# Optimization experiments

Hardware: AMD Instinct MI355X
Metric: run time of the kernel (lower is better)

Reference implementation:

```python
import jax, jax.numpy as jnp
import numpy as np

EPS = 1e-05


def layer_norm(x, scale):
    # Faithful to source bug: returns scale * x_norm + scale (shift param unused)
    mean = jnp.mean(x, axis=-1, keepdims=True)
    var = jnp.var(x, axis=-1, keepdims=True)  # unbiased=False
    x_norm = (x - mean) / jnp.sqrt(var + EPS)
    return scale * x_norm + scale


def mhsa(x, wq, wk, wv, wo, bo, n_heads):
    b, t, d = x.shape
    hd = d // n_heads
    # torch Linear: y = x @ W.T (no qkv bias)
    q = (x @ wq.T).reshape(b, t, n_heads, hd).transpose(0, 2, 1, 3)  # bhtd
    k = (x @ wk.T).reshape(b, t, n_heads, hd).transpose(0, 2, 1, 3)
    v = (x @ wv.T).reshape(b, t, n_heads, hd).transpose(0, 2, 1, 3)
    scores = jnp.einsum('bhqd,bhkd->bhqk', q, k)
    causal = jnp.triu(jnp.ones((t, t), dtype=bool), k=1)
    scores = jnp.where(causal, -jnp.inf, scores)
    attn = jax.nn.softmax(scores / np.sqrt(hd).astype(np.float32), axis=-1)
    ctx = jnp.einsum('bhqk,bhkd->bhqd', attn, v)
    ctx = ctx.transpose(0, 2, 1, 3).reshape(b, t, d)
    return ctx @ wo.T + bo


def setup_inputs() -> dict:
    key = jax.random.key(0)
    ks = jax.random.split(key, 6)
    B, T, D = 2, 2048, 1024
    return {
        'x': jax.random.normal(ks[0], (B, T, D), dtype=jnp.float32),
        'wq': jax.random.normal(ks[1], (D, D), dtype=jnp.float32) * 0.02,
        'wk': jax.random.normal(ks[2], (D, D), dtype=jnp.float32) * 0.02,
        'wv': jax.random.normal(ks[3], (D, D), dtype=jnp.float32) * 0.02,
        'wo': jax.random.normal(ks[4], (D, D), dtype=jnp.float32) * 0.02,
        'bo': jnp.zeros((D,), dtype=jnp.float32),
        'ln1_scale': jnp.ones((D,), dtype=jnp.float32),
        'ln2_scale': jnp.ones((D,), dtype=jnp.float32),
    }


def reference(x, wq, wk, wv, wo, bo, ln1_scale, ln2_scale):
    n_heads = 16
    # Block 1: norm1 -> attn -> (+residual); dropout is identity in eval mode
    h = x + mhsa(layer_norm(x, ln1_scale), wq, wk, wv, wo, bo, n_heads)
    # Block 2: source calls self.attn (same weights) again, not self.ff
    out = h + mhsa(layer_norm(h, ln2_scale), wq, wk, wv, wo, bo, n_heads)
    return out
```

## Files before the change

### kernel.cpp

```cpp
#include <hip/hip_runtime.h>
#include <hip/hip_bf16.h>
#include <math.h>

#define Dm 1024
#define Tm 2048
#define Bm 2
#define Hm 16
#define HDm 64
#define Rm (Bm*Tm)
#define QKS 2048

typedef __attribute__((ext_vector_type(8))) short sh8;
typedef __attribute__((ext_vector_type(4))) float f32x4;

#define AS1(p) ((const __attribute__((address_space(1))) void*)(p))
#define AS3(p) ((__attribute__((address_space(3))) void*)(p))

__device__ __forceinline__ short f2bs(float f) {
    union { float f; unsigned u; } v; v.f = f;
    unsigned r = v.u + 0x7FFFu + ((v.u >> 16) & 1u);
    return (short)(r >> 16);
}

__global__ __launch_bounds__(256) void convert_w(const float* __restrict__ wq,
                                                 const float* __restrict__ wk,
                                                 const float* __restrict__ wv,
                                                 const float* __restrict__ wo,
                                                 short* __restrict__ wqkv,
                                                 short* __restrict__ wob) {
    int idx = (blockIdx.x * 256 + threadIdx.x) * 4;
    const int M1 = 1 << 20;
    const float* src; short* dst; int off;
    if (idx < M1)           { src = wq; dst = wqkv;          off = idx; }
    else if (idx < 2*M1)    { src = wk; dst = wqkv + M1;     off = idx - M1; }
    else if (idx < 3*M1)    { src = wv; dst = wqkv + 2*M1;   off = idx - 2*M1; }
    else                    { src = wo; dst = wob;           off = idx - 3*M1; }
    float4 v = *(const float4*)(src + off);
    short4 o;
    o.x = f2bs(v.x); o.y = f2bs(v.y); o.z = f2bs(v.z); o.w = f2bs(v.w);
    *(short4*)(dst + off) = o;
}

__global__ __launch_bounds__(256) void ln_kernel(const float* __restrict__ x,
                                                 const float* __restrict__ scale,
                                                 short* __restrict__ out) {
    int row = blockIdx.x;
    int t = threadIdx.x;
    const float4* xr = (const float4*)(x + (size_t)row * Dm);
    float4 v = xr[t];
    float s  = v.x + v.y + v.z + v.w;
    float ss = v.x*v.x + v.y*v.y + v.z*v.z + v.w*v.w;
    #pragma unroll
    for (int off = 32; off; off >>= 1) {
        s  += __shfl_xor(s, off);
        ss += __shfl_xor(ss, off);
    }
    __shared__ float red[8];
    int wave = t >> 6, lane = t & 63;
    if (lane == 0) { red[wave*2] = s; red[wave*2+1] = ss; }
    __syncthreads();
    s  = red[0] + red[2] + red[4] + red[6];
    ss = red[1] + red[3] + red[5] + red[7];
    float mean = s * (1.0f / Dm);
    float var  = ss * (1.0f / Dm) - mean * mean;
    float rstd = 1.0f / sqrtf(var + 1e-5f);
    float4 sc = ((const float4*)scale)[t];
    short4 o;
    o.x = f2bs(sc.x * ((v.x - mean) * rstd) + sc.x);
    o.y = f2bs(sc.y * ((v.y - mean) * rstd) + sc.y);
    o.z = f2bs(sc.z * ((v.z - mean) * rstd) + sc.z);
    o.w = f2bs(sc.w * ((v.w - mean) * rstd) + sc.w);
    ((short4*)(out + (size_t)row * Dm))[t] = o;
}

template<int BN, int MODE>
__global__ __launch_bounds__(256) void gemm_mfma(const short* __restrict__ A,
                                                 const short* __restrict__ B,
                                                 const float* __restrict__ bias,
                                                 const float* __restrict__ res,
                                                 void* __restrict__ Cv,
                                                 short* __restrict__ Vt,
                                                 int M, int N, int K) {
    __shared__ short As[128*32];
    __shared__ short Bs[BN*32];
    __shared__ short Tb[(MODE==1) ? 4*16*68 : 4];
    const int NJ = BN / 32;
    int t = threadIdx.x;
    int lane = t & 63, w = t >> 6;
    int l = lane & 15, quad = lane >> 4;
    int wm = (w & 1) * 64, wn = (w >> 1) * (BN/2);
    int m0 = blockIdx.y * 128, n0 = blockIdx.x * BN;

    f32x4 acc[4][NJ];
    #pragma unroll
    for (int i = 0; i < 4; i++)
        #pragma unroll
        for (int j = 0; j < NJ; j++)
            acc[i][j] = (f32x4){0.f,0.f,0.f,0.f};

    for (int k0 = 0; k0 < K; k0 += 32) {
        __syncthreads();
        #pragma unroll
        for (int p = 0; p < 2; p++) {
            int off = p*4096 + t*16;
            int row = off >> 6;
            int c = ((off >> 4) & 3) ^ (row & 3);
            const short* ga = A + (size_t)(m0 + row) * K + k0 + c*8;
            __builtin_amdgcn_global_load_lds(AS1(ga), AS3((char*)As + off), 16, 0, 0);
        }
        #pragma unroll
        for (int p = 0; p < BN/64; p++) {
            int off = p*4096 + t*16;
            int row = off >> 6;
            int c = ((off >> 4) & 3) ^ (row & 3);
            const short* gb = B + (size_t)(n0 + row) * K + k0 + c*8;
            __builtin_amdgcn_global_load_lds(AS1(gb), AS3((char*)Bs + off), 16, 0, 0);
        }
        __syncthreads();
        sh8 af[4], bf[NJ];
        #pragma unroll
        for (int i = 0; i < 4; i++) {
            int m = wm + i*16 + l;
            af[i] = *(const sh8*)((const char*)As + m*64 + ((quad ^ (m & 3)) * 16));
        }
        #pragma unroll
        for (int j = 0; j < NJ; j++) {
            int n = wn + j*16 + l;
            bf[j] = *(const sh8*)((const char*)Bs + n*64 + ((quad ^ (n & 3)) * 16));
        }
        #pragma unroll
        for (int i = 0; i < 4; i++)
            #pragma unroll
            for (int j = 0; j < NJ; j++)
                acc[i][j] = __builtin_amdgcn_mfma_f32_16x16x32_bf16(af[i], bf[j], acc[i][j], 0, 0, 0);
    }
    if (MODE == 0) {
        #pragma unroll
        for (int i = 0; i < 4; i++)
            #pragma unroll
            for (int j = 0; j < NJ; j++)
                #pragma unroll
                for (int r = 0; r < 4; r++) {
                    int m = m0 + wm + i*16 + quad*4 + r;
                    int n = n0 + wn + j*16 + l;
                    float vv = acc[i][j][r] + bias[n] + res[(size_t)m * N + n];
                    ((float*)Cv)[(size_t)m * N + n] = vv;
                }
    } else {
        if (n0 < 2048) {
            #pragma unroll
            for (int i = 0; i < 4; i++)
                #pragma unroll
                for (int j = 0; j < NJ; j++)
                    #pragma unroll
                    for (int r = 0; r < 4; r++) {
                        int m = m0 + wm + i*16 + quad*4 + r;
                        int n = n0 + wn + j*16 + l;
                        ((short*)Cv)[(size_t)m * QKS + n] = f2bs(acc[i][j][r]);
                    }
        } else {
            int bq = m0 >> 11;
            int key0 = (m0 & 2047) + wm;
            int h = (n0 + wn - 2048) >> 6;
            short* vout = Vt + ((size_t)(bq*Hm + h) * HDm) * Tm + key0;
            #pragma unroll
            for (int j = 0; j < NJ; j++) {
                #pragma unroll
                for (int i = 0; i < 4; i++) {
                    short4 o;
                    o.x = f2bs(acc[i][j][0]); o.y = f2bs(acc[i][j][1]);
                    o.z = f2bs(acc[i][j][2]); o.w = f2bs(acc[i][j][3]);
                    *(short4*)&Tb[w*(16*68) + l*68 + i*16 + quad*4] = o;
                }
                #pragma unroll
                for (int st = 0; st < 2; st++) {
                    int rr = st*8 + (lane >> 3);
                    int cc = lane & 7;
                    sh8 vv = *(const sh8*)&Tb[w*(16*68) + rr*68 + cc*8];
                    *(sh8*)(vout + (size_t)(j*16 + rr) * Tm + cc*8) = vv;
                }
            }
        }
    }
}

__device__ __forceinline__ void stage_kv(const short* kp0, const short* vh,
                                         int kbase, short* Kd, short* Vd, int t) {
    #pragma unroll
    for (int p = 0; p < 2; p++) {
        int off = p*4096 + t*16;
        int row = off >> 7;
        int c = ((off >> 4) & 7) ^ (row & 7);
        const short* gk = kp0 + (size_t)(kbase + row) * QKS + c*8;
        __builtin_amdgcn_global_load_lds(AS1(gk), AS3((char*)Kd + off), 16, 0, 0);
        const short* gv = vh + (size_t)row * Tm + kbase + c*8;
        __builtin_amdgcn_global_load_lds(AS1(gv), AS3((char*)Vd + off), 16, 0, 0);
    }
}

__global__ __launch_bounds__(256) void attn_mfma(const short* __restrict__ qk,
                                                 const short* __restrict__ vtg,
                                                 short* __restrict__ ctx) {
    __shared__ short Kl[2][64*64];
    __shared__ short Vl[2][64*64];
    __shared__ short Pl[4][16*64];
    int t = threadIdx.x;
    int lane = t & 63, w = t >> 6;
    int l = lane & 15, quad = lane >> 4;
    int bh = blockIdx.x;
    int xi = blockIdx.y;
    int cc0 = xi & 7, kk0 = xi >> 3;
    int qt = (kk0 == 0) ? cc0 : (kk0 == 1) ? (15 - cc0)
           : (kk0 == 2) ? (16 + cc0) : (31 - cc0);
    int b = bh >> 4, h = bh & 15;
    size_t rbase = (size_t)b * Tm;
    const short* qp0 = qk + rbase * QKS + h*HDm;
    const short* kp0 = qp0 + Dm;
    const short* vh  = vtg + ((size_t)bh * HDm) * Tm;
    int qtbase = qt * 64;

    sh8 qf0, qf1;
    {
        const short* qp = qp0 + (size_t)(qtbase + w*16 + l) * QKS + quad*8;
        qf0 = *(const sh8*)qp;
        qf1 = *(const sh8*)(qp + 32);
    }
    f32x4 O[4] = {{0,0,0,0},{0,0,0,0},{0,0,0,0},{0,0,0,0}};
    float ps[4] = {0.f, 0.f, 0.f, 0.f};

    int cur = 0;
    stage_kv(kp0, vh, 0, Kl[0], Vl[0], t);
    __syncthreads();

    int swl = l & 7;
    for (int kc = 0; kc <= qt; kc++) {
        int kbase = kc * 64;
        if (kc < qt)
            stage_kv(kp0, vh, kbase + 64, Kl[cur^1], Vl[cur^1], t);

        f32x4 S[4];
        #pragma unroll
        for (int kt = 0; kt < 4; kt++) {
            const f32x4 z = {0.f,0.f,0.f,0.f};
            int key = kt*16 + l;
            const char* kb = (const char*)Kl[cur] + key*128;
            int sw = key & 7;
            sh8 k0 = *(const sh8*)(kb + ((quad ^ sw) * 16));
            sh8 k1 = *(const sh8*)(kb + (((4 + quad) ^ sw) * 16));
            f32x4 s = __builtin_amdgcn_mfma_f32_16x16x32_bf16(k0, qf0, z, 0, 0, 0);
            s = __builtin_amdgcn_mfma_f32_16x16x32_bf16(k1, qf1, s, 0, 0, 0);
            S[kt] = s;
        }
        bool needmask = (kbase + 63 > qtbase + w*16);
        int qrow = qtbase + w*16 + l;
        #pragma unroll
        for (int kt = 0; kt < 4; kt++) {
            float p[4];
            if (needmask) {
                #pragma unroll
                for (int r = 0; r < 4; r++) {
                    int key = kbase + kt*16 + quad*4 + r;
                    p[r] = (key > qrow) ? 0.f : __expf(S[kt][r] * 0.125f);
                }
            } else {
                #pragma unroll
                for (int r = 0; r < 4; r++)
                    p[r] = __expf(S[kt][r] * 0.125f);
            }
            ps[kt] += (p[0] + p[1]) + (p[2] + p[3]);
            __hip_bfloat162 pa = __float22bfloat162_rn({p[0], p[1]});
            __hip_bfloat162 pb = __float22bfloat162_rn({p[2], p[3]});
            union { __hip_bfloat162 hh[2]; short4 s4; } u;
            u.hh[0] = pa; u.hh[1] = pb;
            int g = (kt*2 + (quad >> 1)) ^ swl;
            *(short4*)&Pl[w][l*64 + g*8 + (quad & 1)*4] = u.s4;
        }
        sh8 p0 = *(const sh8*)&Pl[w][l*64 + ((quad ^ swl) * 8)];
        sh8 p1 = *(const sh8*)&Pl[w][l*64 + (((4 + quad) ^ swl) * 8)];
        #pragma unroll
        for (int dt = 0; dt < 4; dt++) {
            int d = dt*16 + l;
            const char* vb = (const char*)Vl[cur] + d*128;
            int sw = d & 7;
            sh8 v0 = *(const sh8*)(vb + ((quad ^ sw) * 16));
            sh8 v1 = *(const sh8*)(vb + (((4 + quad) ^ sw) * 16));
            O[dt] = __builtin_amdgcn_mfma_f32_16x16x32_bf16(p0, v0, O[dt], 0, 0, 0);
            O[dt] = __builtin_amdgcn_mfma_f32_16x16x32_bf16(p1, v1, O[dt], 0, 0, 0);
        }
        __syncthreads();
        cur ^= 1;
    }

    float psum = (ps[0] + ps[1]) + (ps[2] + ps[3]);
    psum += __shfl_xor(psum, 16);
    psum += __shfl_xor(psum, 32);
    #pragma unroll
    for (int r = 0; r < 4; r++) {
        int src = (lane & 48) | (((lane >> 4) << 2) + r);
        float inv = 1.0f / __shfl(psum, src);
        int row = qtbase + w*16 + quad*4 + r;
        #pragma unroll
        for (int dt = 0; dt < 4; dt++)
            ctx[(rbase + row) * Dm + h*HDm + dt*16 + l] = f2bs(O[dt][r] * inv);
    }
}

extern "C" void kernel_launch(void* const* d_in, const int* in_sizes, int n_in,
                              void* d_out, int out_size, void* d_ws, size_t ws_size,
                              hipStream_t stream) {
    const float* x   = (const float*)d_in[0];
    const float* wq  = (const float*)d_in[1];
    const float* wk  = (const float*)d_in[2];
    const float* wv  = (const float*)d_in[3];
    const float* wo  = (const float*)d_in[4];
    const float* bo  = (const float*)d_in[5];
    const float* ln1 = (const float*)d_in[6];
    const float* ln2 = (const float*)d_in[7];
    float* out = (float*)d_out;

    short* lnb  = (short*)d_ws;
    short* ctxb = lnb  + (size_t)Rm*Dm;
    short* qk   = ctxb + (size_t)Rm*Dm;
    short* vtg  = qk   + (size_t)Rm*QKS;
    short* wqkv = vtg  + (size_t)Bm*Hm*HDm*Tm;
    short* wob  = wqkv + (size_t)3*Dm*Dm;

    dim3 qgrid(3072/128, Rm/128);
    dim3 pgrid(Dm/64,    Rm/128);
    dim3 agrid(32, 32);

    convert_w<<<4096, 256, 0, stream>>>(wq, wk, wv, wo, wqkv, wob);

    ln_kernel<<<Rm, 256, 0, stream>>>(x, ln1, lnb);
    gemm_mfma<128, 1><<<qgrid, 256, 0, stream>>>(lnb, wqkv, nullptr, nullptr, qk, vtg, Rm, 3072, Dm);
    attn_mfma<<<agrid, 256, 0, stream>>>(qk, vtg, ctxb);
    gemm_mfma<64, 0><<<pgrid, 256, 0, stream>>>(ctxb, wob, bo, x, out, nullptr, Rm, Dm, Dm);

    ln_kernel<<<Rm, 256, 0, stream>>>(out, ln2, lnb);
    gemm_mfma<128, 1><<<qgrid, 256, 0, stream>>>(lnb, wqkv, nullptr, nullptr, qk, vtg, Rm, 3072, Dm);
    attn_mfma<<<agrid, 256, 0, stream>>>(qk, vtg, ctxb);
    gemm_mfma<64, 0><<<pgrid, 256, 0, stream>>>(ctxb, wob, bo, out, out, nullptr, Rm, Dm, Dm);
}
```

Measured before the change: 303.8 us.

## Split long causal attention tiles across two blocks and fold softmax scale into Wq

Query tiles in the upper half of the causal range are split into two key-range halves processed by separate blocks. The partial O and row sums go to fp32 workspace, and a new combine kernel merges them and normalizes. This balances per-block work across the grid (48 vs 32 y-blocks) at the cost of an extra launch and partial-result traffic. The 1/sqrt(hd) scale is folded into the bf16 Wq conversion so the exp skips a multiply, and K/V staging now uses incrementing precomputed pointers. Because there is no max subtraction, the partial sums combine additively.

Result: no change. 309.0 us (+1.7%).

```diff
diff --git a/kernel.cpp b/kernel.cpp
--- a/kernel.cpp
+++ b/kernel.cpp
@@ -30,14 +30,14 @@
                                                  short* __restrict__ wob) {
     int idx = (blockIdx.x * 256 + threadIdx.x) * 4;
     const int M1 = 1 << 20;
-    const float* src; short* dst; int off;
-    if (idx < M1)           { src = wq; dst = wqkv;          off = idx; }
+    const float* src; short* dst; int off; float sc = 1.0f;
+    if (idx < M1)           { src = wq; dst = wqkv;          off = idx; sc = 0.125f; }
     else if (idx < 2*M1)    { src = wk; dst = wqkv + M1;     off = idx - M1; }
     else if (idx < 3*M1)    { src = wv; dst = wqkv + 2*M1;   off = idx - 2*M1; }
     else                    { src = wo; dst = wob;           off = idx - 3*M1; }
     float4 v = *(const float4*)(src + off);
     short4 o;
-    o.x = f2bs(v.x); o.y = f2bs(v.y); o.z = f2bs(v.z); o.w = f2bs(v.w);
+    o.x = f2bs(v.x*sc); o.y = f2bs(v.y*sc); o.z = f2bs(v.z*sc); o.w = f2bs(v.w*sc);
     *(short4*)(dst + off) = o;
 }
 
@@ -184,23 +184,11 @@
     }
 }
 
-__device__ __forceinline__ void stage_kv(const short* kp0, const short* vh,
-                                         int kbase, short* Kd, short* Vd, int t) {
-    #pragma unroll
-    for (int p = 0; p < 2; p++) {
-        int off = p*4096 + t*16;
-        int row = off >> 7;
-        int c = ((off >> 4) & 7) ^ (row & 7);
-        const short* gk = kp0 + (size_t)(kbase + row) * QKS + c*8;
-        __builtin_amdgcn_global_load_lds(AS1(gk), AS3((char*)Kd + off), 16, 0, 0);
-        const short* gv = vh + (size_t)row * Tm + kbase + c*8;
-        __builtin_amdgcn_global_load_lds(AS1(gv), AS3((char*)Vd + off), 16, 0, 0);
-    }
-}
-
 __global__ __launch_bounds__(256) void attn_mfma(const short* __restrict__ qk,
                                                  const short* __restrict__ vtg,
-                                                 short* __restrict__ ctx) {
+                                                 short* __restrict__ ctx,
+                                                 float* __restrict__ opart,
+                                                 float* __restrict__ pspart) {
     __shared__ short Kl[2][64*64];
     __shared__ short Vl[2][64*64];
     __shared__ short Pl[4][16*64];
@@ -208,10 +196,15 @@
     int lane = t & 63, w = t >> 6;
     int l = lane & 15, quad = lane >> 4;
     int bh = blockIdx.x;
-    int xi = blockIdx.y;
-    int cc0 = xi & 7, kk0 = xi >> 3;
-    int qt = (kk0 == 0) ? cc0 : (kk0 == 1) ? (15 - cc0)
-           : (kk0 == 2) ? (16 + cc0) : (31 - cc0);
+    int y  = blockIdx.y;
+    int qt, kc0, kc1, part; bool split;
+    if (y < 16) { qt = y; kc0 = 0; kc1 = qt + 1; part = 0; split = false; }
+    else {
+        int z = y - 16;
+        qt = 16 + (z >> 1); part = z & 1;
+        int n = qt + 1, half = (n + 1) >> 1;
+        kc0 = part ? half : 0; kc1 = part ? n : half; split = true;
+    }
     int b = bh >> 4, h = bh & 15;
     size_t rbase = (size_t)b * Tm;
     const short* qp0 = qk + rbase * QKS + h*HDm;
@@ -228,15 +221,32 @@
     f32x4 O[4] = {{0,0,0,0},{0,0,0,0},{0,0,0,0},{0,0,0,0}};
     float ps[4] = {0.f, 0.f, 0.f, 0.f};
 
+    int offA = t*16, offB = 4096 + t*16;
+    int rowA = offA >> 7, rowB = offB >> 7;
+    int swA = ((offA >> 4) & 7) ^ (rowA & 7);
+    int swB = ((offB >> 4) & 7) ^ (rowB & 7);
+    const short* gkA = kp0 + (size_t)(kc0*64 + rowA) * QKS + swA*8;
+    const short* gkB = kp0 + (size_t)(kc0*64 + rowB) * QKS + swB*8;
+    const short* gvA = vh + (size_t)rowA * Tm + kc0*64 + swA*8;
+    const short* gvB = vh + (size_t)rowB * Tm + kc0*64 + swB*8;
+
+#define STAGE(KD, VD) do { \
+    __builtin_amdgcn_global_load_lds(AS1(gkA), AS3((char*)(KD) + offA), 16, 0, 0); \
+    __builtin_amdgcn_global_load_lds(AS1(gkB), AS3((char*)(KD) + offB), 16, 0, 0); \
+    __builtin_amdgcn_global_load_lds(AS1(gvA), AS3((char*)(VD) + offA), 16, 0, 0); \
+    __builtin_amdgcn_global_load_lds(AS1(gvB), AS3((char*)(VD) + offB), 16, 0, 0); \
+    gkA += 64*QKS; gkB += 64*QKS; gvA += 64; gvB += 64; } while (0)
+
+    STAGE(Kl[0], Vl[0]);
+    __syncthreads();
+
+    int swl = l & 7;
     int cur = 0;
-    stage_kv(kp0, vh, 0, Kl[0], Vl[0], t);
-    __syncthreads();
-
-    int swl = l & 7;
-    for (int kc = 0; kc <= qt; kc++) {
+    for (int kc = kc0; kc < kc1; kc++) {
         int kbase = kc * 64;
-        if (kc < qt)
-            stage_kv(kp0, vh, kbase + 64, Kl[cur^1], Vl[cur^1], t);
+        if (kc + 1 < kc1) {
+            if (cur) STAGE(Kl[0], Vl[0]); else STAGE(Kl[1], Vl[1]);
+        }
 
         f32x4 S[4];
         #pragma unroll
@@ -260,12 +270,12 @@
                 #pragma unroll
                 for (int r = 0; r < 4; r++) {
                     int key = kbase + kt*16 + quad*4 + r;
-                    p[r] = (key > qrow) ? 0.f : __expf(S[kt][r] * 0.125f);
+                    p[r] = (key > qrow) ? 0.f : __expf(S[kt][r]);
                 }
             } else {
                 #pragma unroll
                 for (int r = 0; r < 4; r++)
-                    p[r] = __expf(S[kt][r] * 0.125f);
+                    p[r] = __expf(S[kt][r]);
             }
             ps[kt] += (p[0] + p[1]) + (p[2] + p[3]);
             __hip_bfloat162 pa = __float22bfloat162_rn({p[0], p[1]});
@@ -290,18 +300,60 @@
         __syncthreads();
         cur ^= 1;
     }
+#undef STAGE
 
     float psum = (ps[0] + ps[1]) + (ps[2] + ps[3]);
     psum += __shfl_xor(psum, 16);
     psum += __shfl_xor(psum, 32);
+    if (!split) {
+        #pragma unroll
+        for (int r = 0; r < 4; r++) {
+            int src = (lane & 48) | (((lane >> 4) << 2) + r);
+            float inv = 1.0f / __shfl(psum, src);
+            int row = qtbase + w*16 + quad*4 + r;
+            #pragma unroll
+            for (int dt = 0; dt < 4; dt++)
+                ctx[(rbase + row) * Dm + h*HDm + dt*16 + l] = f2bs(O[dt][r] * inv);
+        }
+    } else {
+        int tile = (bh*16 + (qt - 16)) * 2 + part;
+        float* ob = opart + (size_t)tile * 4096;
+        #pragma unroll
+        for (int r = 0; r < 4; r++) {
+            int row = w*16 + quad*4 + r;
+            #pragma unroll
+            for (int dt = 0; dt < 4; dt++)
+                ob[row*64 + dt*16 + l] = O[dt][r];
+        }
+        if (quad == 0) pspart[tile*64 + w*16 + l] = psum;
+    }
+}
+
+__global__ __launch_bounds__(256) void attn_combine(const float* __restrict__ opart,
+                                                    const float* __restrict__ pspart,
+                                                    short* __restrict__ ctx) {
+    int bh = blockIdx.x;
+    int q16 = blockIdx.y;
+    int b = bh >> 4, h = bh & 15;
+    int t = threadIdx.x;
+    int row = t >> 2;
+    int d0 = (t & 3) * 16;
+    int tile0 = (bh*16 + q16) * 2;
+    const float* o0 = opart + (size_t)tile0 * 4096 + row*64 + d0;
+    const float* o1 = o0 + 4096;
+    float psv = pspart[tile0*64 + row] + pspart[(tile0+1)*64 + row];
+    float inv = 1.0f / psv;
+    short* cp = ctx + ((size_t)(b*Tm + (16+q16)*64 + row)) * Dm + h*HDm + d0;
     #pragma unroll
-    for (int r = 0; r < 4; r++) {
-        int src = (lane & 48) | (((lane >> 4) << 2) + r);
-        float inv = 1.0f / __shfl(psum, src);
-        int row = qtbase + w*16 + quad*4 + r;
-        #pragma unroll
-        for (int dt = 0; dt < 4; dt++)
-            ctx[(rbase + row) * Dm + h*HDm + dt*16 + l] = f2bs(O[dt][r] * inv);
+    for (int j = 0; j < 16; j += 4) {
+        float4 a = *(const float4*)(o0 + j);
+        float4 c = *(const float4*)(o1 + j);
+        short4 o;
+        o.x = f2bs((a.x + c.x) * inv);
+        o.y = f2bs((a.y + c.y) * inv);
+        o.z = f2bs((a.z + c.z) * inv);
+        o.w = f2bs((a.w + c.w) * inv);
+        *(short4*)(cp + j) = o;
     }
 }
 
@@ -324,20 +376,25 @@
     short* vtg  = qk   + (size_t)Rm*QKS;
     short* wqkv = vtg  + (size_t)Bm*Hm*HDm*Tm;
     short* wob  = wqkv + (size_t)3*Dm*Dm;
+    float* opart  = (float*)(wob + (size_t)Dm*Dm);
+    float* pspart = opart + (size_t)32*16*2*4096;
 
     dim3 qgrid(3072/128, Rm/128);
     dim3 pgrid(Dm/64,    Rm/128);
-    dim3 agrid(32, 32);
+    dim3 agrid(32, 48);
+    dim3 cgrid(32, 16);
 
     convert_w<<<4096, 256, 0, stream>>>(wq, wk, wv, wo, wqkv, wob);
 
     ln_kernel<<<Rm, 256, 0, stream>>>(x, ln1, lnb);
     gemm_mfma<128, 1><<<qgrid, 256, 0, stream>>>(lnb, wqkv, nullptr, nullptr, qk, vtg, Rm, 3072, Dm);
-    attn_mfma<<<agrid, 256, 0, stream>>>(qk, vtg, ctxb);
+    attn_mfma<<<agrid, 256, 0, stream>>>(qk, vtg, ctxb, opart, pspart);
+    attn_combine<<<cgrid, 256, 0, stream>>>(opart, pspart, ctxb);
     gemm_mfma<64, 0><<<pgrid, 256, 0, stream>>>(ctxb, wob, bo, x, out, nullptr, Rm, Dm, Dm);
 
     ln_kernel<<<Rm, 256, 0, stream>>>(out, ln2, lnb);
     gemm_mfma<128, 1><<<qgrid, 256, 0, stream>>>(lnb, wqkv, nullptr, nullptr, qk, vtg, Rm, 3072, Dm);
-    attn_mfma<<<agrid, 256, 0, stream>>>(qk, vtg, ctxb);
+    attn_mfma<<<agrid, 256, 0, stream>>>(qk, vtg, ctxb, opart, pspart);
+    attn_combine<<<cgrid, 256, 0, stream>>>(opart, pspart, ctxb);
     gemm_mfma<64, 0><<<pgrid, 256, 0, stream>>>(ctxb, wob, bo, out, out, nullptr, Rm, Dm, Dm);
 }
```

## Rewrite attention with 32x32 MFMA tiles, register-resident P, and folded softmax scale

Applied to the files above, without the earlier changes.

The attention kernel now uses 32x32x16 bf16 MFMA instructions with two waves of 32 query rows each, and 128 threads per block instead of 256. The probability tile stays in registers as the A operand of the PV MFMA, so the per-wave LDS round trip for P goes away. The 1/sqrt(hd) scale is folded into Wq during weight conversion, which removes a multiply before every exp. The V-transpose store order in the QKV GEMM epilogue is permuted to match the new operand layout. Halving the threads per block lowers per-block parallelism and may change occupancy, and pre-scaling Wq before bf16 rounding slightly changes numerics.

Result: no change. 299.6 us (-1.4%).

```diff
diff --git a/kernel.cpp b/kernel.cpp
--- a/kernel.cpp
+++ b/kernel.cpp
@@ -12,6 +12,7 @@
 
 typedef __attribute__((ext_vector_type(8))) short sh8;
 typedef __attribute__((ext_vector_type(4))) float f32x4;
+typedef __attribute__((ext_vector_type(16))) float f32x16;
 
 #define AS1(p) ((const __attribute__((address_space(1))) void*)(p))
 #define AS3(p) ((__attribute__((address_space(3))) void*)(p))
@@ -30,14 +31,14 @@
                                                  short* __restrict__ wob) {
     int idx = (blockIdx.x * 256 + threadIdx.x) * 4;
     const int M1 = 1 << 20;
-    const float* src; short* dst; int off;
-    if (idx < M1)           { src = wq; dst = wqkv;          off = idx; }
+    const float* src; short* dst; int off; float sc = 1.0f;
+    if (idx < M1)           { src = wq; dst = wqkv;          off = idx; sc = 0.125f; }
     else if (idx < 2*M1)    { src = wk; dst = wqkv + M1;     off = idx - M1; }
     else if (idx < 3*M1)    { src = wv; dst = wqkv + 2*M1;   off = idx - 2*M1; }
     else                    { src = wo; dst = wob;           off = idx - 3*M1; }
     float4 v = *(const float4*)(src + off);
     short4 o;
-    o.x = f2bs(v.x); o.y = f2bs(v.y); o.z = f2bs(v.z); o.w = f2bs(v.w);
+    o.x = f2bs(v.x*sc); o.y = f2bs(v.y*sc); o.z = f2bs(v.z*sc); o.w = f2bs(v.w*sc);
     *(short4*)(dst + off) = o;
 }
 
@@ -162,6 +163,7 @@
             int bq = m0 >> 11;
             int key0 = (m0 & 2047) + wm;
             int h = (n0 + wn - 2048) >> 6;
+            int quad2 = ((quad & 1) << 1) | (quad >> 1);
             short* vout = Vt + ((size_t)(bq*Hm + h) * HDm) * Tm + key0;
             #pragma unroll
             for (int j = 0; j < NJ; j++) {
@@ -170,7 +172,7 @@
                     short4 o;
                     o.x = f2bs(acc[i][j][0]); o.y = f2bs(acc[i][j][1]);
                     o.z = f2bs(acc[i][j][2]); o.w = f2bs(acc[i][j][3]);
-                    *(short4*)&Tb[w*(16*68) + l*68 + i*16 + quad*4] = o;
+                    *(short4*)&Tb[w*(16*68) + l*68 + i*16 + quad2*4] = o;
                 }
                 #pragma unroll
                 for (int st = 0; st < 2; st++) {
@@ -184,29 +186,14 @@
     }
 }
 
-__device__ __forceinline__ void stage_kv(const short* kp0, const short* vh,
-                                         int kbase, short* Kd, short* Vd, int t) {
-    #pragma unroll
-    for (int p = 0; p < 2; p++) {
-        int off = p*4096 + t*16;
-        int row = off >> 7;
-        int c = ((off >> 4) & 7) ^ (row & 7);
-        const short* gk = kp0 + (size_t)(kbase + row) * QKS + c*8;
-        __builtin_amdgcn_global_load_lds(AS1(gk), AS3((char*)Kd + off), 16, 0, 0);
-        const short* gv = vh + (size_t)row * Tm + kbase + c*8;
-        __builtin_amdgcn_global_load_lds(AS1(gv), AS3((char*)Vd + off), 16, 0, 0);
-    }
-}
-
-__global__ __launch_bounds__(256) void attn_mfma(const short* __restrict__ qk,
+__global__ __launch_bounds__(128) void attn_mfma(const short* __restrict__ qk,
                                                  const short* __restrict__ vtg,
                                                  short* __restrict__ ctx) {
     __shared__ short Kl[2][64*64];
     __shared__ short Vl[2][64*64];
-    __shared__ short Pl[4][16*64];
     int t = threadIdx.x;
     int lane = t & 63, w = t >> 6;
-    int l = lane & 15, quad = lane >> 4;
+    int l31 = lane & 31, hi = lane >> 5;
     int bh = blockIdx.x;
     int xi = blockIdx.y;
     int cc0 = xi & 7, kk0 = xi >> 3;
@@ -218,90 +205,130 @@
     const short* kp0 = qp0 + Dm;
     const short* vh  = vtg + ((size_t)bh * HDm) * Tm;
     int qtbase = qt * 64;
-
-    sh8 qf0, qf1;
+    int qrow = qtbase + w*32 + l31;
+
+    sh8 qf[4];
     {
-        const short* qp = qp0 + (size_t)(qtbase + w*16 + l) * QKS + quad*8;
-        qf0 = *(const sh8*)qp;
-        qf1 = *(const sh8*)(qp + 32);
-    }
-    f32x4 O[4] = {{0,0,0,0},{0,0,0,0},{0,0,0,0},{0,0,0,0}};
-    float ps[4] = {0.f, 0.f, 0.f, 0.f};
+        const short* qp = qp0 + (size_t)qrow * QKS + hi*8;
+        qf[0] = *(const sh8*)qp;
+        qf[1] = *(const sh8*)(qp + 16);
+        qf[2] = *(const sh8*)(qp + 32);
+        qf[3] = *(const sh8*)(qp + 48);
+    }
+
+    f32x16 O0, O1;
+    #pragma unroll
+    for (int i = 0; i < 16; i++) { O0[i] = 0.f; O1[i] = 0.f; }
+    float ps = 0.f;
+
+    int trow = t >> 3;
+    int c8 = ((t & 7) ^ (trow & 7)) * 8;
+    int ldsoff = t * 16;
+    const short* gk0 = kp0 + (size_t)trow * QKS + c8;
+    const short* gk1 = gk0 + (size_t)16*QKS;
+    const short* gk2 = gk0 + (size_t)32*QKS;
+    const short* gk3 = gk0 + (size_t)48*QKS;
+    const short* gv0 = vh + (size_t)trow * Tm + c8;
+    const short* gv1 = gv0 + (size_t)16*Tm;
+    const short* gv2 = gv0 + (size_t)32*Tm;
+    const short* gv3 = gv0 + (size_t)48*Tm;
+
+#define STAGE(KD, VD) do { \
+    __builtin_amdgcn_global_load_lds(AS1(gk0), AS3((char*)(KD) + ldsoff), 16, 0, 0); \
+    __builtin_amdgcn_global_load_lds(AS1(gk1), AS3((char*)(KD) + 2048 + ldsoff), 16, 0, 0); \
+    __builtin_amdgcn_global_load_lds(AS1(gk2), AS3((char*)(KD) + 4096 + ldsoff), 16, 0, 0); \
+    __builtin_amdgcn_global_load_lds(AS1(gk3), AS3((char*)(KD) + 6144 + ldsoff), 16, 0, 0); \
+    __builtin_amdgcn_global_load_lds(AS1(gv0), AS3((char*)(VD) + ldsoff), 16, 0, 0); \
+    __builtin_amdgcn_global_load_lds(AS1(gv1), AS3((char*)(VD) + 2048 + ldsoff), 16, 0, 0); \
+    __builtin_amdgcn_global_load_lds(AS1(gv2), AS3((char*)(VD) + 4096 + ldsoff), 16, 0, 0); \
+    __builtin_amdgcn_global_load_lds(AS1(gv3), AS3((char*)(VD) + 6144 + ldsoff), 16, 0, 0); \
+    gk0 += (size_t)64*QKS; gk1 += (size_t)64*QKS; gk2 += (size_t)64*QKS; gk3 += (size_t)64*QKS; \
+    gv0 += 64; gv1 += 64; gv2 += 64; gv3 += 64; } while (0)
+
+    STAGE(Kl[0], Vl[0]);
+    __syncthreads();
 
     int cur = 0;
-    stage_kv(kp0, vh, 0, Kl[0], Vl[0], t);
-    __syncthreads();
-
-    int swl = l & 7;
     for (int kc = 0; kc <= qt; kc++) {
         int kbase = kc * 64;
-        if (kc < qt)
-            stage_kv(kp0, vh, kbase + 64, Kl[cur^1], Vl[cur^1], t);
-
-        f32x4 S[4];
-        #pragma unroll
-        for (int kt = 0; kt < 4; kt++) {
-            const f32x4 z = {0.f,0.f,0.f,0.f};
-            int key = kt*16 + l;
-            const char* kb = (const char*)Kl[cur] + key*128;
+        if (kc < qt) {
+            if (cur) STAGE(Kl[0], Vl[0]); else STAGE(Kl[1], Vl[1]);
+        }
+
+        const char* Kb = (const char*)Kl[cur];
+        bool needmask = (kbase + 63 > qtbase + w*32);
+        sh8 pa[4];
+        #pragma unroll
+        for (int kt = 0; kt < 2; kt++) {
+            int key = kt*32 + l31;
+            const char* kr = Kb + key*128;
             int sw = key & 7;
-            sh8 k0 = *(const sh8*)(kb + ((quad ^ sw) * 16));
-            sh8 k1 = *(const sh8*)(kb + (((4 + quad) ^ sw) * 16));
-            f32x4 s = __builtin_amdgcn_mfma_f32_16x16x32_bf16(k0, qf0, z, 0, 0, 0);
-            s = __builtin_amdgcn_mfma_f32_16x16x32_bf16(k1, qf1, s, 0, 0, 0);
-            S[kt] = s;
-        }
-        bool needmask = (kbase + 63 > qtbase + w*16);
-        int qrow = qtbase + w*16 + l;
-        #pragma unroll
-        for (int kt = 0; kt < 4; kt++) {
-            float p[4];
+            f32x16 c;
+            #pragma unroll
+            for (int i = 0; i < 16; i++) c[i] = 0.f;
+            #pragma unroll
+            for (int s = 0; s < 4; s++) {
+                sh8 kf = *(const sh8*)(kr + (((s*2 + hi) ^ sw) * 16));
+                c = __builtin_amdgcn_mfma_f32_32x32x16_bf16(kf, qf[s], c, 0, 0, 0);
+            }
+            float p_[16];
             if (needmask) {
                 #pragma unroll
-                for (int r = 0; r < 4; r++) {
-                    int key = kbase + kt*16 + quad*4 + r;
-                    p[r] = (key > qrow) ? 0.f : __expf(S[kt][r] * 0.125f);
+                for (int r = 0; r < 16; r++) {
+                    int key_r = kbase + kt*32 + (r&3) + 8*(r>>2) + 4*hi;
+                    p_[r] = (key_r > qrow) ? 0.f : __expf(c[r]);
                 }
             } else {
                 #pragma unroll
-                for (int r = 0; r < 4; r++)
-                    p[r] = __expf(S[kt][r] * 0.125f);
-            }
-            ps[kt] += (p[0] + p[1]) + (p[2] + p[3]);
-            __hip_bfloat162 pa = __float22bfloat162_rn({p[0], p[1]});
-            __hip_bfloat162 pb = __float22bfloat162_rn({p[2], p[3]});
-            union { __hip_bfloat162 hh[2]; short4 s4; } u;
-            u.hh[0] = pa; u.hh[1] = pb;
-            int g = (kt*2 + (quad >> 1)) ^ swl;
-            *(short4*)&Pl[w][l*64 + g*8 + (quad & 1)*4] = u.s4;
-        }
-        sh8 p0 = *(const sh8*)&Pl[w][l*64 + ((quad ^ swl) * 8)];
-        sh8 p1 = *(const sh8*)&Pl[w][l*64 + (((4 + quad) ^ swl) * 8)];
-        #pragma unroll
-        for (int dt = 0; dt < 4; dt++) {
-            int d = dt*16 + l;
-            const char* vb = (const char*)Vl[cur] + d*128;
+                for (int r = 0; r < 16; r++) p_[r] = __expf(c[r]);
+            }
+            ps += (((p_[0]+p_[1])+(p_[2]+p_[3])) + ((p_[4]+p_[5])+(p_[6]+p_[7])))
+                + (((p_[8]+p_[9])+(p_[10]+p_[11])) + ((p_[12]+p_[13])+(p_[14]+p_[15])));
+            #pragma unroll
+            for (int gg = 0; gg < 2; gg++) {
+                union { __hip_bfloat162 h2[4]; sh8 s8; } u;
+                u.h2[0] = __float22bfloat162_rn({p_[gg*8+0], p_[gg*8+1]});
+                u.h2[1] = __float22bfloat162_rn({p_[gg*8+2], p_[gg*8+3]});
+                u.h2[2] = __float22bfloat162_rn({p_[gg*8+4], p_[gg*8+5]});
+                u.h2[3] = __float22bfloat162_rn({p_[gg*8+6], p_[gg*8+7]});
+                pa[kt*2 + gg] = u.s8;
+            }
+        }
+        const char* Vb = (const char*)Vl[cur];
+        {
+            int d = l31;
+            const char* vr = Vb + d*128;
             int sw = d & 7;
-            sh8 v0 = *(const sh8*)(vb + ((quad ^ sw) * 16));
-            sh8 v1 = *(const sh8*)(vb + (((4 + quad) ^ sw) * 16));
-            O[dt] = __builtin_amdgcn_mfma_f32_16x16x32_bf16(p0, v0, O[dt], 0, 0, 0);
-            O[dt] = __builtin_amdgcn_mfma_f32_16x16x32_bf16(p1, v1, O[dt], 0, 0, 0);
+            #pragma unroll
+            for (int G = 0; G < 4; G++) {
+                sh8 vf = *(const sh8*)(vr + (((G*2 + hi) ^ sw) * 16));
+                O0 = __builtin_amdgcn_mfma_f32_32x32x16_bf16(pa[G], vf, O0, 0, 0, 0);
+            }
+        }
+        {
+            int d = 32 + l31;
+            const char* vr = Vb + d*128;
+            int sw = d & 7;
+            #pragma unroll
+            for (int G = 0; G < 4; G++) {
+                sh8 vf = *(const sh8*)(vr + (((G*2 + hi) ^ sw) * 16));
+                O1 = __builtin_amdgcn_mfma_f32_32x32x16_bf16(pa[G], vf, O1, 0, 0, 0);
+            }
         }
         __syncthreads();
         cur ^= 1;
     }
-
-    float psum = (ps[0] + ps[1]) + (ps[2] + ps[3]);
-    psum += __shfl_xor(psum, 16);
-    psum += __shfl_xor(psum, 32);
+#undef STAGE
+
+    ps += __shfl_xor(ps, 32);
+    float inv_own = 1.0f / ps;
+    short* cp = ctx + (rbase + qtbase + w*32) * Dm + h*HDm + l31;
     #pragma unroll
-    for (int r = 0; r < 4; r++) {
-        int src = (lane & 48) | (((lane >> 4) << 2) + r);
-        float inv = 1.0f / __shfl(psum, src);
-        int row = qtbase + w*16 + quad*4 + r;
-        #pragma unroll
-        for (int dt = 0; dt < 4; dt++)
-            ctx[(rbase + row) * Dm + h*HDm + dt*16 + l] = f2bs(O[dt][r] * inv);
+    for (int r = 0; r < 16; r++) {
+        int rl = (r&3) + 8*(r>>2) + 4*hi;
+        float inv = __shfl(inv_own, rl);
+        cp[(size_t)rl * Dm]      = f2bs(O0[r] * inv);
+        cp[(size_t)rl * Dm + 32] = f2bs(O1[r] * inv);
     }
 }
 
@@ -333,11 +360,11 @@
 
     ln_kernel<<<Rm, 256, 0, stream>>>(x, ln1, lnb);
     gemm_mfma<128, 1><<<qgrid, 256, 0, stream>>>(lnb, wqkv, nullptr, nullptr, qk, vtg, Rm, 3072, Dm);
-    attn_mfma<<<agrid, 256, 0, stream>>>(qk, vtg, ctxb);
+    attn_mfma<<<agrid, 128, 0, stream>>>(qk, vtg, ctxb);
     gemm_mfma<64, 0><<<pgrid, 256, 0, stream>>>(ctxb, wob, bo, x, out, nullptr, Rm, Dm, Dm);
 
     ln_kernel<<<Rm, 256, 0, stream>>>(out, ln2, lnb);
     gemm_mfma<128, 1><<<qgrid, 256, 0, stream>>>(lnb, wqkv, nullptr, nullptr, qk, vtg, Rm, 3072, Dm);
-    attn_mfma<<<agrid, 256, 0, stream>>>(qk, vtg, ctxb);
+    attn_mfma<<<agrid, 128, 0, stream>>>(qk, vtg, ctxb);
     gemm_mfma<64, 0><<<pgrid, 256, 0, stream>>>(ctxb, wob, bo, out, out, nullptr, Rm, Dm, Dm);
 }
```
